# Kernel tuning notes

Hardware: AMD Instinct MI355X
Metric: run time of the kernel (lower is better)

## Reference

```python
import jax, jax.numpy as jnp
import numpy as np


def setup_inputs() -> dict:
    key = jax.random.key(0)
    ks = jax.random.split(key, 12)
    B, N, Din, D, K = 2, 1024, 64, 64, 24
    s = lambda fan_in: 1.0 / np.sqrt(fan_in)
    return {
        "feature": jax.random.normal(ks[0], (B, N, Din), jnp.float32),
        "xyz": jax.random.normal(ks[1], (B, N, 3), jnp.float32),
        "pw1": jax.random.uniform(ks[2], (Din, D), jnp.float32, -s(Din), s(Din)),
        "pb1": jax.random.uniform(ks[3], (D,), jnp.float32, -s(Din), s(Din)),
        "pw2": jax.random.uniform(ks[4], (D, D), jnp.float32, -s(D), s(D)),
        "pb2": jax.random.uniform(ks[5], (D,), jnp.float32, -s(D), s(D)),
        "rw": jax.random.uniform(ks[6], (3, D * D), jnp.float32, -s(3), s(3)),
        "rb": jax.random.uniform(ks[7], (D * D,), jnp.float32, -s(3), s(3)),
        "sw": jax.random.uniform(ks[8], (D, D), jnp.float32, -s(D), s(D)),
        "sb": jax.random.uniform(ks[9], (D,), jnp.float32, -s(D), s(D)),
        "knn_num": 24,
    }


def reference(feature, xyz, pw1, pb1, pw2, pb2, rw, rb, sw, sb, knn_num):
    B, N, _ = feature.shape
    D = pw2.shape[1]
    K = knn_num
    # KNN over xyz (squared euclidean distances, smallest K)
    sq = jnp.sum(xyz * xyz, axis=-1)  # [B,N]
    d2 = sq[:, :, None] + sq[:, None, :] - 2.0 * jnp.einsum('bnc,bmc->bnm', xyz, xyz)
    _, idx = jax.lax.top_k(-d2, K)  # [B,N,K]
    bidx = jnp.arange(B)[:, None, None]
    rel = xyz[bidx, idx] - xyz[:, :, None, :]  # [B,N,K,3]
    # prefix MLP: relu(Linear -> ReLU -> Linear)
    feat = jax.nn.relu(jax.nn.relu(feature @ pw1 + pb1) @ pw2 + pb2)  # [B,N,D]
    # per-edge weight generation + softmax over (K*D)
    w = (rel @ rw + rb).reshape(B, N, K * D, D)
    w = jax.nn.softmax(w, axis=-2)
    # gather neighbor features and aggregate
    gv = feat[bidx, idx].reshape(B, N, K * D)  # [B,N,K*D]
    out = jnp.einsum('bnm,bnmd->bnd', gv, w)  # [B,N,D]
    out = out @ sw + sb
    return (out, N)
```

## Files before the change

kernel.cpp:

```cpp
#include <hip/hip_runtime.h>
#include <math.h>

#define BB 2
#define NN 1024
#define DD 64
#define KK 24
#define NPTS (BB * NN)

#if __has_builtin(__builtin_amdgcn_exp2f)
#define EXP2(x) __builtin_amdgcn_exp2f(x)
#else
#define EXP2(x) exp2f(x)
#endif

typedef float v2f __attribute__((ext_vector_type(2)));


__global__ __launch_bounds__(256) void prep_mlp_knn_kernel(
    const float* __restrict__ feature, const float* __restrict__ xyz,
    const float* __restrict__ pw1, const float* __restrict__ pb1,
    const float* __restrict__ pw2, const float* __restrict__ pb2,
    const float* __restrict__ rw, const float* __restrict__ rb,
    float* __restrict__ feat, int* __restrict__ idx_out,
    float* __restrict__ rwS, float* __restrict__ rbS) {
    int bid = blockIdx.x;
    int tid = threadIdx.x;

    if (bid < 512) {
        int r = tid >> 6;
        int d = tid & 63;
        int row = bid * 4 + r;
        __shared__ float s_in[4][64];
        __shared__ float s_h[4][64];
        s_in[r][d] = feature[row * 64 + d];
        __syncthreads();
        float h = pb1[d];
#pragma unroll
        for (int i = 0; i < 64; i++) h = __builtin_fmaf(s_in[r][i], pw1[i * 64 + d], h);
        h = fmaxf(h, 0.f);
        s_h[r][d] = h;
        __syncthreads();
        float f = pb2[d];
#pragma unroll
        for (int i = 0; i < 64; i++) f = __builtin_fmaf(s_h[r][i], pw2[i * 64 + d], f);
        f = fmaxf(f, 0.f);
        feat[row * 64 + d] = f;
    } else if (bid < 528) {
        const float LOG2E = 1.4426950408889634f;
        int t = (bid - 512) * 256 + tid;
#pragma unroll
        for (int q = 0; q < 4; q++) {
            int i = t + q * 4096;
            rwS[i] = rw[i] * LOG2E;
        }
        rbS[t] = rb[t] * LOG2E;
    } else {
        int w = tid >> 6;
        int lane = tid & 63;
        int pt = (bid - 528) * 4 + w;
        int b = pt >> 10;
        int n = pt & 1023;
        const float* xb = xyz + (size_t)b * NN * 3;
        float xn = xb[n * 3 + 0], yn = xb[n * 3 + 1], zn = xb[n * 3 + 2];
        float sqn = xn * xn + yn * yn + zn * zn;
        float dist[16];
#pragma unroll
        for (int c = 0; c < 16; c++) {
            int m = c * 64 + lane;
            float xm = xb[m * 3 + 0], ym = xb[m * 3 + 1], zm = xb[m * 3 + 2];
            float sqm = xm * xm + ym * ym + zm * zm;
            float dot = xn * xm + yn * ym + zn * zm;
            dist[c] = sqn + sqm - 2.0f * dot;
        }
        for (int r = 0; r < KK; r++) {
            float best = 3.4e38f;
            int bi = 1 << 30;
#pragma unroll
            for (int c = 0; c < 16; c++) {
                if (dist[c] < best) {
                    best = dist[c];
                    bi = c * 64 + lane;
                }
            }
#pragma unroll
            for (int off = 32; off >= 1; off >>= 1) {
                float ob = __shfl_down(best, off);
                int oi = __shfl_down(bi, off);
                if (ob < best || (ob == best && oi < bi)) {
                    best = ob;
                    bi = oi;
                }
            }
            bi = __shfl(bi, 0);
            if ((bi & 63) == lane) dist[bi >> 6] = 3.4e38f;
            if (lane == 0) idx_out[pt * KK + r] = bi;
        }
    }
}

#define GVS 28
__global__ __launch_bounds__(256) void agg_kernel(const float* __restrict__ xyz,
                                                  const float* __restrict__ feat,
                                                  const int* __restrict__ idx,
                                                  const float* __restrict__ rwS,
                                                  const float* __restrict__ rbS,
                                                  const float* __restrict__ sw,
                                                  const float* __restrict__ sb,
                                                  float* __restrict__ out) {
    int pt = blockIdx.x;
    int b = pt >> 10;
    int n = pt & 1023;
    int tid = threadIdx.x;
    int w = tid >> 6;
    int d = tid & 63;

    __shared__ float s_rel[KK][3];
    __shared__ __align__(16) float s_gvt[64][GVS];
    __shared__ float s_red[8][64];
    __shared__ float s_pre[64];

    const float* xb = xyz + (size_t)b * NN * 3;
    if (tid < KK * 3) {
        int k = tid / 3, c = tid % 3;
        int nb = idx[pt * KK + k];
        s_rel[k][c] = xb[nb * 3 + c] - xb[n * 3 + c];
    }
    for (int t = tid; t < KK * 64; t += 256) {
        int k = t >> 6, j = t & 63;
        int nb = idx[pt * KK + k];
        s_gvt[j][k] = feat[((size_t)b * NN + nb) * 64 + j];
    }
    __syncthreads();

    v2f rx[12], ry[12], rz[12];
#pragma unroll
    for (int k = 0; k < 12; k++) {
        rx[k] = (v2f){s_rel[2 * k][0], s_rel[2 * k + 1][0]};
        ry[k] = (v2f){s_rel[2 * k][1], s_rel[2 * k + 1][1]};
        rz[k] = (v2f){s_rel[2 * k][2], s_rel[2 * k + 1][2]};
    }

    v2f l0 = {0.f, 0.f}, l1 = {0.f, 0.f}, a0 = {0.f, 0.f}, a1 = {0.f, 0.f};
    for (int jj = 0; jj < 16; jj++) {
        int j = w * 16 + jj;
        int col = j * 64 + d;
        float r0 = rwS[col];
        float r1 = rwS[4096 + col];
        float r2 = rwS[8192 + col];
        float rbv = rbS[col];
        v2f R0 = {r0, r0}, R1 = {r1, r1}, R2 = {r2, r2}, RB = {rbv, rbv};
        const float4* g4 = (const float4*)(&s_gvt[j][0]);
#pragma unroll
        for (int q = 0; q < 6; q++) {
            float4 g = g4[q];
            v2f ga = {g.x, g.y};
            v2f gb = {g.z, g.w};
            v2f t0 = rx[2 * q] * R0 + (ry[2 * q] * R1 + (rz[2 * q] * R2 + RB));
            v2f t1 = rx[2 * q + 1] * R0 + (ry[2 * q + 1] * R1 + (rz[2 * q + 1] * R2 + RB));
            v2f e0 = {EXP2(t0.x), EXP2(t0.y)};
            v2f e1 = {EXP2(t1.x), EXP2(t1.y)};
            l0 += e0;
            l1 += e1;
            a0 += ga * e0;
            a1 += gb * e1;
        }
    }
    s_red[w][d] = l0.x + l0.y + l1.x + l1.y;
    s_red[4 + w][d] = a0.x + a0.y + a1.x + a1.y;
    __syncthreads();
    if (tid < 64) {
        float L = s_red[0][d] + s_red[1][d] + s_red[2][d] + s_red[3][d];
        float A = s_red[4][d] + s_red[5][d] + s_red[6][d] + s_red[7][d];
        s_pre[d] = A / L;
    }
    __syncthreads();
    float part = 0.f;
#pragma unroll
    for (int dd = 0; dd < 16; dd++) {
        int drow = w * 16 + dd;
        part = __builtin_fmaf(s_pre[drow], sw[drow * 64 + d], part);
    }
    s_red[w][d] = part;
    __syncthreads();
    if (tid < 64) {
        float o = s_red[0][d] + s_red[1][d] + s_red[2][d] + s_red[3][d] + sb[d];
        out[(size_t)pt * 64 + d] = o;
    }
    if (pt == 0 && tid == 0) out[(size_t)NPTS * 64] = 1024.0f;
}

extern "C" void kernel_launch(void* const* d_in, const int* in_sizes, int n_in,
                              void* d_out, int out_size, void* d_ws, size_t ws_size,
                              hipStream_t stream) {
    const float* feature = (const float*)d_in[0];
    const float* xyz = (const float*)d_in[1];
    const float* pw1 = (const float*)d_in[2];
    const float* pb1 = (const float*)d_in[3];
    const float* pw2 = (const float*)d_in[4];
    const float* pb2 = (const float*)d_in[5];
    const float* rw = (const float*)d_in[6];
    const float* rb = (const float*)d_in[7];
    const float* sw = (const float*)d_in[8];
    const float* sb = (const float*)d_in[9];
    float* out = (float*)d_out;

    char* ws = (char*)d_ws;
    float* feat = (float*)(ws);
    int* idx = (int*)(ws + 524288);
    float* rwS = (float*)(ws + 720896);
    float* rbS = (float*)(ws + 770048);

    prep_mlp_knn_kernel<<<1040, 256, 0, stream>>>(feature, xyz, pw1, pb1, pw2, pb2,
                                                  rw, rb, feat, idx, rwS, rbS);
    agg_kernel<<<NPTS, 256, 0, stream>>>(xyz, feat, idx, rwS, rbS, sw, sb, out);
}
```

Before: 139.2 us.

## Pack edge-weight params as float4, prefetch next row, force packed FMA asm

The three rw rows and the rb bias are interleaved into one float4 per column, so the aggregation loop issues one 16-byte load instead of four scalar loads. The next column's float4 is prefetched one iteration ahead to hide global latency. Inline asm forces v_pk_fma_f32 and v_pk_add_f32 for the logit and accumulation math so the compiler cannot fall back to scalar ops. The asm blocks the compiler from scheduling around these instructions, and the float4 layout uses 16-byte loads with a 16-byte stride across lanes.

Measured after the change: 132.9 us. -4.5%, faster.

```diff
diff --git a/kernel.cpp b/kernel.cpp
--- a/kernel.cpp
+++ b/kernel.cpp
@@ -14,6 +14,17 @@
 #endif
 
 typedef float v2f __attribute__((ext_vector_type(2)));
+
+static __device__ __forceinline__ v2f pk_fma(v2f a, v2f b, v2f c) {
+    v2f d;
+    asm("v_pk_fma_f32 %0, %1, %2, %3" : "=v"(d) : "v"(a), "v"(b), "v"(c));
+    return d;
+}
+static __device__ __forceinline__ v2f pk_add(v2f a, v2f b) {
+    v2f d;
+    asm("v_pk_add_f32 %0, %1, %2" : "=v"(d) : "v"(a), "v"(b));
+    return d;
+}
 
 
 __global__ __launch_bounds__(256) void prep_mlp_knn_kernel(
@@ -22,7 +33,7 @@
     const float* __restrict__ pw2, const float* __restrict__ pb2,
     const float* __restrict__ rw, const float* __restrict__ rb,
     float* __restrict__ feat, int* __restrict__ idx_out,
-    float* __restrict__ rwS, float* __restrict__ rbS) {
+    float4* __restrict__ rwP) {
     int bid = blockIdx.x;
     int tid = threadIdx.x;
 
@@ -48,12 +59,12 @@
     } else if (bid < 528) {
         const float LOG2E = 1.4426950408889634f;
         int t = (bid - 512) * 256 + tid;
-#pragma unroll
-        for (int q = 0; q < 4; q++) {
-            int i = t + q * 4096;
-            rwS[i] = rw[i] * LOG2E;
-        }
-        rbS[t] = rb[t] * LOG2E;
+        float4 v;
+        v.x = rw[t] * LOG2E;
+        v.y = rw[4096 + t] * LOG2E;
+        v.z = rw[8192 + t] * LOG2E;
+        v.w = rb[t] * LOG2E;
+        rwP[t] = v;
     } else {
         int w = tid >> 6;
         int lane = tid & 63;
@@ -102,8 +113,7 @@
 __global__ __launch_bounds__(256) void agg_kernel(const float* __restrict__ xyz,
                                                   const float* __restrict__ feat,
                                                   const int* __restrict__ idx,
-                                                  const float* __restrict__ rwS,
-                                                  const float* __restrict__ rbS,
+                                                  const float4* __restrict__ rwP,
                                                   const float* __restrict__ sw,
                                                   const float* __restrict__ sb,
                                                   float* __restrict__ out) {
@@ -141,29 +151,29 @@
     }
 
     v2f l0 = {0.f, 0.f}, l1 = {0.f, 0.f}, a0 = {0.f, 0.f}, a1 = {0.f, 0.f};
+    int col0 = (w * 16) * 64 + d;
+    float4 rv = rwP[col0];
     for (int jj = 0; jj < 16; jj++) {
         int j = w * 16 + jj;
-        int col = j * 64 + d;
-        float r0 = rwS[col];
-        float r1 = rwS[4096 + col];
-        float r2 = rwS[8192 + col];
-        float rbv = rbS[col];
-        v2f R0 = {r0, r0}, R1 = {r1, r1}, R2 = {r2, r2}, RB = {rbv, rbv};
+        float4 rvn = rv;
+        if (jj < 15) rvn = rwP[col0 + (jj + 1) * 64];
+        v2f R0 = {rv.x, rv.x}, R1 = {rv.y, rv.y}, R2 = {rv.z, rv.z}, RB = {rv.w, rv.w};
         const float4* g4 = (const float4*)(&s_gvt[j][0]);
 #pragma unroll
         for (int q = 0; q < 6; q++) {
             float4 g = g4[q];
             v2f ga = {g.x, g.y};
             v2f gb = {g.z, g.w};
-            v2f t0 = rx[2 * q] * R0 + (ry[2 * q] * R1 + (rz[2 * q] * R2 + RB));
-            v2f t1 = rx[2 * q + 1] * R0 + (ry[2 * q + 1] * R1 + (rz[2 * q + 1] * R2 + RB));
+            v2f t0 = pk_fma(rx[2 * q], R0, pk_fma(ry[2 * q], R1, pk_fma(rz[2 * q], R2, RB)));
+            v2f t1 = pk_fma(rx[2 * q + 1], R0, pk_fma(ry[2 * q + 1], R1, pk_fma(rz[2 * q + 1], R2, RB)));
             v2f e0 = {EXP2(t0.x), EXP2(t0.y)};
             v2f e1 = {EXP2(t1.x), EXP2(t1.y)};
-            l0 += e0;
-            l1 += e1;
-            a0 += ga * e0;
-            a1 += gb * e1;
+            l0 = pk_add(l0, e0);
+            l1 = pk_add(l1, e1);
+            a0 = pk_fma(ga, e0, a0);
+            a1 = pk_fma(gb, e1, a1);
         }
+        rv = rvn;
     }
     s_red[w][d] = l0.x + l0.y + l1.x + l1.y;
     s_red[4 + w][d] = a0.x + a0.y + a1.x + a1.y;
@@ -207,10 +217,9 @@
     char* ws = (char*)d_ws;
     float* feat = (float*)(ws);
     int* idx = (int*)(ws + 524288);
-    float* rwS = (float*)(ws + 720896);
-    float* rbS = (float*)(ws + 770048);
+    float4* rwP = (float4*)(ws + 720896);
 
     prep_mlp_knn_kernel<<<1040, 256, 0, stream>>>(feature, xyz, pw1, pb1, pw2, pb2,
-                                                  rw, rb, feat, idx, rwS, rbS);
-    agg_kernel<<<NPTS, 256, 0, stream>>>(xyz, feat, idx, rwS, rbS, sw, sb, out);
-}
+                                                  rw, rb, feat, idx, rwP);
+    agg_kernel<<<NPTS, 256, 0, stream>>>(xyz, feat, idx, rwP, sw, sb, out);
+}
```

## Move edge-weight generation and aggregation onto bf16 MFMA matrix instructions

Applied to the files above, without the earlier changes.

The aggregation kernel is rewritten so that the per-edge logits (rel·rw + rb) are computed with a 32x32x16 bf16 MFMA, with the bias folded in through a constant-one column. The exponentials are packed to bf16 in shared memory, and the weighted sum plus the softmax denominator are computed with 16x16x32 bf16 MFMAs using an extra row of ones. rw/rb are pre-packed into interleaved bf16 in the prep kernel. This aims to remove the scalar FMA and exp-accumulate VALU work, but lowers precision to bf16 for weights, relative positions, features and exponentials, and adds shared-memory traffic and extra barriers.

After: 138.5 us. About the same (-0.5%).

```diff
diff --git a/kernel.cpp b/kernel.cpp
--- a/kernel.cpp
+++ b/kernel.cpp
@@ -13,7 +13,20 @@
 #define EXP2(x) exp2f(x)
 #endif
 
-typedef float v2f __attribute__((ext_vector_type(2)));
+typedef short short8 __attribute__((ext_vector_type(8)));
+typedef float floatx16 __attribute__((ext_vector_type(16)));
+typedef float floatx4 __attribute__((ext_vector_type(4)));
+
+static __device__ __forceinline__ unsigned short bf_rne(float x) {
+    unsigned u = __float_as_uint(x);
+    u += 0x7FFFu + ((u >> 16) & 1u);
+    return (unsigned short)(u >> 16);
+}
+static __device__ __forceinline__ unsigned bfpack(float hi, float lo) {
+    return __builtin_amdgcn_perm(__float_as_uint(hi), __float_as_uint(lo), 0x07060302u);
+}
+
+union U8 { unsigned u[4]; short8 s8; };
 
 
 __global__ __launch_bounds__(256) void prep_mlp_knn_kernel(
@@ -22,7 +35,7 @@
     const float* __restrict__ pw2, const float* __restrict__ pb2,
     const float* __restrict__ rw, const float* __restrict__ rb,
     float* __restrict__ feat, int* __restrict__ idx_out,
-    float* __restrict__ rwS, float* __restrict__ rbS) {
+    unsigned short* __restrict__ rwB) {
     int bid = blockIdx.x;
     int tid = threadIdx.x;
 
@@ -48,12 +61,14 @@
     } else if (bid < 528) {
         const float LOG2E = 1.4426950408889634f;
         int t = (bid - 512) * 256 + tid;
-#pragma unroll
-        for (int q = 0; q < 4; q++) {
-            int i = t + q * 4096;
-            rwS[i] = rw[i] * LOG2E;
-        }
-        rbS[t] = rb[t] * LOG2E;
+        unsigned b0 = bf_rne(rw[t] * LOG2E);
+        unsigned b1 = bf_rne(rw[4096 + t] * LOG2E);
+        unsigned b2 = bf_rne(rw[8192 + t] * LOG2E);
+        unsigned b3 = bf_rne(rb[t] * LOG2E);
+        uint2 v;
+        v.x = b0 | (b1 << 16);
+        v.y = b2 | (b3 << 16);
+        *(uint2*)(rwB + 4 * t) = v;
     } else {
         int w = tid >> 6;
         int lane = tid & 63;
@@ -98,93 +113,139 @@
     }
 }
 
-#define GVS 28
-__global__ __launch_bounds__(256) void agg_kernel(const float* __restrict__ xyz,
-                                                  const float* __restrict__ feat,
-                                                  const int* __restrict__ idx,
-                                                  const float* __restrict__ rwS,
-                                                  const float* __restrict__ rbS,
-                                                  const float* __restrict__ sw,
-                                                  const float* __restrict__ sb,
-                                                  float* __restrict__ out) {
+__global__ __launch_bounds__(256, 4) void agg_kernel(const float* __restrict__ xyz,
+                                                     const float* __restrict__ feat,
+                                                     const int* __restrict__ idx,
+                                                     const unsigned short* __restrict__ rwB,
+                                                     const float* __restrict__ sw,
+                                                     const float* __restrict__ sb,
+                                                     float* __restrict__ out) {
     int pt = blockIdx.x;
     int b = pt >> 10;
     int n = pt & 1023;
     int tid = threadIdx.x;
     int w = tid >> 6;
-    int d = tid & 63;
-
-    __shared__ float s_rel[KK][3];
-    __shared__ __align__(16) float s_gvt[64][GVS];
-    __shared__ float s_red[8][64];
+    int lane = tid & 63;
+    int n16 = lane & 15, q4 = lane >> 4;
+    int n32 = lane & 31, h = lane >> 5;
+
+    __shared__ unsigned short s_et[64][196];
+    __shared__ unsigned short s_gv[KK * 64];
+    __shared__ unsigned short s_rel4[32][4];
     __shared__ float s_pre[64];
+    __shared__ float s_red[4][64];
 
     const float* xb = xyz + (size_t)b * NN * 3;
-    if (tid < KK * 3) {
-        int k = tid / 3, c = tid % 3;
+
+    if (tid < 32) {
+        if (tid < KK) {
+            int nb = idx[pt * KK + tid];
+            s_rel4[tid][0] = bf_rne(xb[nb * 3 + 0] - xb[n * 3 + 0]);
+            s_rel4[tid][1] = bf_rne(xb[nb * 3 + 1] - xb[n * 3 + 1]);
+            s_rel4[tid][2] = bf_rne(xb[nb * 3 + 2] - xb[n * 3 + 2]);
+            s_rel4[tid][3] = 0x3F80;
+        } else {
+            s_rel4[tid][0] = 0; s_rel4[tid][1] = 0; s_rel4[tid][2] = 0; s_rel4[tid][3] = 0;
+        }
+    }
+#pragma unroll
+    for (int i = 0; i < 6; i++) {
+        int flat = tid + 256 * i;
+        int j = flat / 24;
+        int k = flat - 24 * j;
         int nb = idx[pt * KK + k];
-        s_rel[k][c] = xb[nb * 3 + c] - xb[n * 3 + c];
-    }
-    for (int t = tid; t < KK * 64; t += 256) {
-        int k = t >> 6, j = t & 63;
-        int nb = idx[pt * KK + k];
-        s_gvt[j][k] = feat[((size_t)b * NN + nb) * 64 + j];
+        s_gv[flat] = bf_rne(feat[((size_t)b * NN + nb) * 64 + j]);
     }
     __syncthreads();
 
-    v2f rx[12], ry[12], rz[12];
-#pragma unroll
-    for (int k = 0; k < 12; k++) {
-        rx[k] = (v2f){s_rel[2 * k][0], s_rel[2 * k + 1][0]};
-        ry[k] = (v2f){s_rel[2 * k][1], s_rel[2 * k + 1][1]};
-        rz[k] = (v2f){s_rel[2 * k][2], s_rel[2 * k + 1][2]};
-    }
-
-    v2f l0 = {0.f, 0.f}, l1 = {0.f, 0.f}, a0 = {0.f, 0.f}, a1 = {0.f, 0.f};
-    for (int jj = 0; jj < 16; jj++) {
-        int j = w * 16 + jj;
-        int col = j * 64 + d;
-        float r0 = rwS[col];
-        float r1 = rwS[4096 + col];
-        float r2 = rwS[8192 + col];
-        float rbv = rbS[col];
-        v2f R0 = {r0, r0}, R1 = {r1, r1}, R2 = {r2, r2}, RB = {rbv, rbv};
-        const float4* g4 = (const float4*)(&s_gvt[j][0]);
-#pragma unroll
-        for (int q = 0; q < 6; q++) {
-            float4 g = g4[q];
-            v2f ga = {g.x, g.y};
-            v2f gb = {g.z, g.w};
-            v2f t0 = rx[2 * q] * R0 + (ry[2 * q] * R1 + (rz[2 * q] * R2 + RB));
-            v2f t1 = rx[2 * q + 1] * R0 + (ry[2 * q + 1] * R1 + (rz[2 * q + 1] * R2 + RB));
-            v2f e0 = {EXP2(t0.x), EXP2(t0.y)};
-            v2f e1 = {EXP2(t1.x), EXP2(t1.y)};
-            l0 += e0;
-            l1 += e1;
-            a0 += ga * e0;
-            a1 += gb * e1;
-        }
-    }
-    s_red[w][d] = l0.x + l0.y + l1.x + l1.y;
-    s_red[4 + w][d] = a0.x + a0.y + a1.x + a1.y;
+    short8 afrag;
+    {
+        unsigned a01 = 0, a23 = 0;
+        if (h == 0) {
+            const unsigned* p = (const unsigned*)&s_rel4[n32][0];
+            a01 = p[0];
+            a23 = p[1];
+        }
+        U8 u; u.u[0] = a01; u.u[1] = a23; u.u[2] = 0; u.u[3] = 0;
+        afrag = u.s8;
+    }
+
+    floatx4 c2 = (floatx4)(0.0f);
+    const floatx16 z16 = (floatx16)(0.0f);
+    const unsigned ONES = 0x3F803F80u;
+
+    for (int c = 0; c < 8; c++) {
+        int nt0 = 16 * c + 4 * w;
+        uint2 gb = *(const uint2*)(rwB + 4 * ((nt0 << 5) + n32));
+#pragma unroll 1
+        for (int t = 0; t < 4; t++) {
+            int nt = nt0 + t;
+            uint2 gbn = gb;
+            if (t < 3) gbn = *(const uint2*)(rwB + 4 * (((nt + 1) << 5) + n32));
+            short8 bfrag;
+            {
+                unsigned b01 = (h == 0) ? gb.x : 0u;
+                unsigned b23 = (h == 0) ? gb.y : 0u;
+                U8 u; u.u[0] = b01; u.u[1] = b23; u.u[2] = 0; u.u[3] = 0;
+                bfrag = u.s8;
+            }
+            floatx16 acc = __builtin_amdgcn_mfma_f32_32x32x16_bf16(afrag, bfrag, z16, 0, 0, 0);
+            int jl = (nt >> 1) - 8 * c;
+            int d = ((nt & 1) << 5) + n32;
+#pragma unroll
+            for (int g = 0; g < 3; g++) {
+                float e0 = EXP2(acc[4 * g + 0]);
+                float e1 = EXP2(acc[4 * g + 1]);
+                float e2 = EXP2(acc[4 * g + 2]);
+                float e3 = EXP2(acc[4 * g + 3]);
+                uint2 pv;
+                pv.x = bfpack(e1, e0);
+                pv.y = bfpack(e3, e2);
+                int mm = jl * 24 + 8 * g + 4 * h;
+                *(uint2*)&s_et[d][mm] = pv;
+            }
+            gb = gbn;
+        }
+        __syncthreads();
+#pragma unroll
+        for (int ks = 0; ks < 6; ks++) {
+            int mmb = 32 * ks + 8 * q4;
+            uint4 gvv = *(const uint4*)&s_gv[192 * c + mmb];
+            short8 ag;
+            {
+                U8 u;
+                u.u[0] = (n16 == 0) ? gvv.x : ((n16 == 1) ? ONES : 0u);
+                u.u[1] = (n16 == 0) ? gvv.y : ((n16 == 1) ? ONES : 0u);
+                u.u[2] = (n16 == 0) ? gvv.z : ((n16 == 1) ? ONES : 0u);
+                u.u[3] = (n16 == 0) ? gvv.w : ((n16 == 1) ? ONES : 0u);
+                ag = u.s8;
+            }
+            const unsigned short* ep = &s_et[16 * w + n16][mmb];
+            uint2 e01 = *(const uint2*)(ep);
+            uint2 e23 = *(const uint2*)(ep + 4);
+            short8 bg;
+            {
+                U8 u; u.u[0] = e01.x; u.u[1] = e01.y; u.u[2] = e23.x; u.u[3] = e23.y;
+                bg = u.s8;
+            }
+            c2 = __builtin_amdgcn_mfma_f32_16x16x32_bf16(ag, bg, c2, 0, 0, 0);
+        }
+        __syncthreads();
+    }
+
+    if (q4 == 0) s_pre[16 * w + n16] = c2[0] / c2[1];
+    __syncthreads();
+    float part = 0.f;
+#pragma unroll
+    for (int i = 0; i < 16; i++) {
+        int r = 16 * w + i;
+        part = __builtin_fmaf(s_pre[r], sw[r * 64 + lane], part);
+    }
+    s_red[w][lane] = part;
     __syncthreads();
     if (tid < 64) {
-        float L = s_red[0][d] + s_red[1][d] + s_red[2][d] + s_red[3][d];
-        float A = s_red[4][d] + s_red[5][d] + s_red[6][d] + s_red[7][d];
-        s_pre[d] = A / L;
-    }
-    __syncthreads();
-    float part = 0.f;
-#pragma unroll
-    for (int dd = 0; dd < 16; dd++) {
-        int drow = w * 16 + dd;
-        part = __builtin_fmaf(s_pre[drow], sw[drow * 64 + d], part);
-    }
-    s_red[w][d] = part;
-    __syncthreads();
-    if (tid < 64) {
-        float o = s_red[0][d] + s_red[1][d] + s_red[2][d] + s_red[3][d] + sb[d];
-        out[(size_t)pt * 64 + d] = o;
+        float o = s_red[0][tid] + s_red[1][tid] + s_red[2][tid] + s_red[3][tid] + sb[tid];
+        out[(size_t)pt * 64 + tid] = o;
     }
     if (pt == 0 && tid == 0) out[(size_t)NPTS * 64] = 1024.0f;
 }
@@ -207,10 +268,9 @@
     char* ws = (char*)d_ws;
     float* feat = (float*)(ws);
     int* idx = (int*)(ws + 524288);
-    float* rwS = (float*)(ws + 720896);
-    float* rbS = (float*)(ws + 770048);
+    unsigned short* rwB = (unsigned short*)(ws + 720896);
 
     prep_mlp_knn_kernel<<<1040, 256, 0, stream>>>(feature, xyz, pw1, pb1, pw2, pb2,
-                                                  rw, rb, feat, idx, rwS, rbS);
-    agg_kernel<<<NPTS, 256, 0, stream>>>(xyz, feat, idx, rwS, rbS, sw, sb, out);
-}
+                                                  rw, rb, feat, idx, rwB);
+    agg_kernel<<<NPTS, 256, 0, stream>>>(xyz, feat, idx, rwB, sw, sb, out);
+}
```
